# Kernel tuning notes

Hardware: AMD Instinct MI355X
Metric: run time of the kernel (lower is better)

## Reference

```python
import jax, jax.numpy as jnp
import numpy as np

N = 100000
E = 3200000
D = 256
HOPS = 3  # K + 1


def setup_inputs() -> dict:
    key = jax.random.key(0)
    k1, k2, k3, k4, k5 = jax.random.split(key, 5)
    node_features = jax.random.normal(k1, (N, D), dtype=jnp.float32)
    # glorot-uniform-like scale for K+1 Dense kernels
    limit = np.sqrt(6.0 / (D + D)).astype(np.float32)
    W = jax.random.uniform(k2, (HOPS, D, D), dtype=jnp.float32, minval=-limit, maxval=limit)
    adj_vals = jax.random.uniform(k3, (HOPS, E), dtype=jnp.float32)
    adj_rows = jax.random.randint(k4, (HOPS, E), 0, N, dtype=jnp.int32)
    adj_cols = jax.random.randint(k5, (HOPS, E), 0, N, dtype=jnp.int32)
    return {"node_features": node_features, "W": W, "adj_vals": adj_vals,
            "adj_rows": adj_rows, "adj_cols": adj_cols}


def reference(node_features, W, adj_vals, adj_rows, adj_cols):
    """Faithful eval-mode forward: sum over hops of SpMM(A_hop, X @ W_hop), then ReLU.
    Dropout is identity at inference (training=False)."""
    n = node_features.shape[0]
    out = jnp.zeros((n, W.shape[-1]), dtype=node_features.dtype)
    for hop in range(W.shape[0]):  # small fixed K+1 loop, structurally distinct hops
        feats = node_features @ W[hop]                      # [N, out_dim]
        msgs = adj_vals[hop][:, None] * feats[adj_cols[hop]]  # gather + scale, [E, out_dim]
        out = out + jax.ops.segment_sum(msgs, adj_rows[hop], num_segments=n)
    return jax.nn.relu(out)
```

## Files before the change

kernel.cpp:

```cpp
#include <hip/hip_runtime.h>

#define D 256
#define MAXKEY 1600
#define PCH 32768

typedef __attribute__((ext_vector_type(8))) short short8;
typedef __attribute__((ext_vector_type(4))) float f32x4;

__device__ __forceinline__ ushort f2b(float f) {
    unsigned u = __float_as_uint(f);
    u += 0x7fffu + ((u >> 16) & 1u);
    return (ushort)(u >> 16);
}
__device__ __forceinline__ float b2f(ushort h) {
    return __uint_as_float(((unsigned)h) << 16);
}
__device__ __forceinline__ long long ntload_ll(const void* p) {
    return __builtin_nontemporal_load((const long long*)p);
}

__global__ void zero_int_kernel(int* __restrict__ p, int n) {
    int stride = gridDim.x * blockDim.x;
    for (int i = blockIdx.x * blockDim.x + threadIdx.x; i < n; i += stride) p[i] = 0;
}

__global__ void xconv_kernel(const float* __restrict__ X, ushort* __restrict__ Xb, int total8) {
    int i = blockIdx.x * 256 + threadIdx.x;
    if (i >= total8) return;
    const float4 a = *(const float4*)(X + (size_t)i * 8);
    const float4 b = *(const float4*)(X + (size_t)i * 8 + 4);
    ushort o8[8] = {f2b(a.x), f2b(a.y), f2b(a.z), f2b(a.w),
                    f2b(b.x), f2b(b.y), f2b(b.z), f2b(b.w)};
    *(short8*)(Xb + (size_t)i * 8) = *(const short8*)o8;
}

__global__ void wconv_kernel(const float* __restrict__ W, ushort* __restrict__ WT, int total) {
    int idx = blockIdx.x * 256 + threadIdx.x;
    if (idx >= total) return;
    int h = idx >> 16;
    int c = (idx >> 8) & 255, k = idx & 255;
    WT[(h << 16) + c * 256 + k] = f2b(W[(h << 16) + k * 256 + c]);
}

__global__ __launch_bounds__(256) void bhist_kernel(const int* __restrict__ rows,
                                                    int* __restrict__ bhistG, int e, int nbuk) {
    __shared__ int lh[MAXKEY];
    int h = blockIdx.y;
    const int* r = rows + (size_t)h * e;
    for (int k = threadIdx.x; k < nbuk; k += 256) lh[k] = 0;
    __syncthreads();
    int stride = gridDim.x * 256;
    for (int i = blockIdx.x * 256 + threadIdx.x; i < e; i += stride)
        atomicAdd(&lh[r[i] >> 6], 1);
    __syncthreads();
    int* g = bhistG + (size_t)h * nbuk;
    for (int k = threadIdx.x; k < nbuk; k += 256)
        if (lh[k]) atomicAdd(&g[k], lh[k]);
}

__global__ __launch_bounds__(1024) void bscan_kernel(const int* __restrict__ bhistG,
                                                     int* __restrict__ gbase,
                                                     int* __restrict__ gcur, int total) {
    __shared__ int s[1024];
    int t = threadIdx.x;
    int C = (total + 1023) >> 10;
    int i0 = t * C, i1 = min(i0 + C, total);
    int sum = 0;
    for (int i = i0; i < i1; ++i) sum += bhistG[i];
    s[t] = sum;
    __syncthreads();
    for (int off = 1; off < 1024; off <<= 1) {
        int x = (t >= off) ? s[t - off] : 0;
        __syncthreads();
        s[t] += x;
        __syncthreads();
    }
    int run = s[t] - sum;
    for (int i = i0; i < i1; ++i) {
        gbase[i] = run; gcur[i] = run;
        run += bhistG[i];
    }
    if (t == 1023) gbase[total] = s[1023];
}

__global__ __launch_bounds__(256) void bpart_kernel(const int* __restrict__ rows,
                                                    const int* __restrict__ cols,
                                                    const float* __restrict__ vals,
                                                    int* __restrict__ gcur, int2* __restrict__ raw,
                                                    int e, int nbuk) {
    __shared__ int lbase[MAXKEY];
    __shared__ int lcur[MAXKEY];
    int h = blockIdx.y;
    const int*   rr = rows + (size_t)h * e;
    const int*   cc = cols + (size_t)h * e;
    const float* vv = vals + (size_t)h * e;
    int c0 = blockIdx.x * PCH;
    int c1 = min(c0 + PCH, e);
    if (c0 >= c1) return;
    for (int k = threadIdx.x; k < nbuk; k += 256) { lbase[k] = 0; lcur[k] = 0; }
    __syncthreads();
    for (int i = c0 + threadIdx.x; i < c1; i += 256)
        atomicAdd(&lbase[rr[i] >> 6], 1);
    __syncthreads();
    int* gc = gcur + (size_t)h * nbuk;
    for (int k = threadIdx.x; k < nbuk; k += 256) {
        int c = lbase[k];
        lbase[k] = c ? atomicAdd(&gc[k], c) : 0;
    }
    __syncthreads();
    for (int i = c0 + threadIdx.x; i < c1; i += 256) {
        int row = rr[i];
        int p = lbase[row >> 6] + atomicAdd(&lcur[row >> 6], 1);
        raw[p] = make_int2(cc[i] | ((row & 63) << 24), __float_as_int(vv[i]));
    }
}

__global__ __launch_bounds__(256) void bsort_kernel(const int* __restrict__ gbase,
                                                    const int2* __restrict__ raw,
                                                    int2* __restrict__ eg,
                                                    int* __restrict__ row_ptr,
                                                    int n, int nbuk) {
    __shared__ int hist[64], excl[64], cur[64];
    int key = blockIdx.x;
    int h = key / nbuk, b = key % nbuk;
    int s = gbase[key], t = gbase[key + 1];
    int tid = threadIdx.x;
    if (tid < 64) hist[tid] = 0;
    __syncthreads();
    for (int i = s + tid; i < t; i += 256)
        atomicAdd(&hist[(((unsigned)raw[i].x) >> 24) & 63], 1);
    __syncthreads();
    if (tid == 0) {
        int run = s;
        for (int j = 0; j < 64; ++j) { excl[j] = run; cur[j] = run; run += hist[j]; }
    }
    __syncthreads();
    int* rp = row_ptr + (size_t)h * (n + 1);
    if (tid < 64) {
        int grow = b * 64 + tid;
        if (grow < n) rp[grow] = excl[tid];
    }
    if (tid == 0 && b == nbuk - 1) rp[n] = t;
    for (int i = s + tid; i < t; i += 256) {
        int2 ev = raw[i];
        int j = (((unsigned)ev.x) >> 24) & 63;
        int p = atomicAdd(&cur[j], 1);
        eg[p] = ev;
    }
}

__global__ __launch_bounds__(256) void spmmX_kernel(const int* __restrict__ rp,
                                                    const int2* __restrict__ eg,
                                                    const ushort* __restrict__ Xb,
                                                    ushort* __restrict__ Yh, int n) {
    int w = threadIdx.x >> 6, lane = threadIdx.x & 63;
    int r = blockIdx.x * 4 + w;
    if (r >= n) return;
    int half = lane >> 5, l5 = lane & 31;
    int doff = l5 * 8;
    int e0 = rp[r], e1 = rp[r + 1];
    float acc[8] = {};
    int m0 = e0 + half, m1 = e0 + 2 + half;
    long long ev0 = (m0 < e1) ? ntload_ll(eg + m0) : 0;
    long long ev1 = (m1 < e1) ? ntload_ll(eg + m1) : 0;
    for (int ee = e0; ee < e1; ee += 4) {
        long long c0 = ev0, c1 = ev1;
        int n0 = ee + 4 + half, n1 = ee + 6 + half;
        ev0 = (n0 < e1) ? ntload_ll(eg + n0) : 0;
        ev1 = (n1 < e1) ? ntload_ll(eg + n1) : 0;
        int col0 = ((int)(unsigned)c0) & 0xFFFFFF;
        int col1 = ((int)(unsigned)c1) & 0xFFFFFF;
        short8 v0 = *(const short8*)(Xb + (size_t)col0 * 256 + doff);
        short8 v1 = *(const short8*)(Xb + (size_t)col1 * 256 + doff);
        float val0 = __int_as_float((int)(c0 >> 32));
        float val1 = __int_as_float((int)(c1 >> 32));
        #pragma unroll
        for (int i = 0; i < 8; ++i)
            acc[i] = fmaf(val0, b2f((ushort)v0[i]), acc[i]);
        #pragma unroll
        for (int i = 0; i < 8; ++i)
            acc[i] = fmaf(val1, b2f((ushort)v1[i]), acc[i]);
    }
    #pragma unroll
    for (int i = 0; i < 8; ++i)
        acc[i] += __shfl_xor(acc[i], 32);
    if (half == 0) {
        union { ushort u[8]; long long ll[2]; } o;
        #pragma unroll
        for (int i = 0; i < 8; ++i) o.u[i] = f2b(acc[i]);
        long long* dst = (long long*)(Yh + (size_t)r * 256 + doff);
        __builtin_nontemporal_store(o.ll[0], dst);
        __builtin_nontemporal_store(o.ll[1], dst + 1);
    }
}

#define APAD 40

__global__ __launch_bounds__(256) void gemmY_kernel(const ushort* __restrict__ Y,
                                                    const ushort* __restrict__ WT,
                                                    float* __restrict__ out, int M,
                                                    int nh, int mode) {
    __shared__ ushort As[64 * APAD];
    __shared__ ushort Bs[64 * APAD];
    int tid = threadIdx.x;
    int r0 = blockIdx.x * 64, c0 = blockIdx.y * 64;
    int w = tid >> 6, lane = tid & 63;
    int wr = w >> 1, wc = w & 1;
    int lo = lane & 15, hi = lane >> 4;
    f32x4 acc[2][2] = {};
    int srow = tid >> 2;
    int skoff = (tid & 3) * 8;
    int arow = r0 + srow; if (arow > M - 1) arow = M - 1;
    for (int h = 0; h < nh; ++h) {
        const ushort* ap = Y + ((size_t)h * M + arow) * 256 + skoff;
        const ushort* bp = WT + ((size_t)h << 16) + (size_t)(c0 + srow) * 256 + skoff;
        for (int kk = 0; kk < 256; kk += 32) {
            short8 av = *(const short8*)(ap + kk);
            short8 bv = *(const short8*)(bp + kk);
            __syncthreads();
            *(short8*)&As[srow * APAD + skoff] = av;
            *(short8*)&Bs[srow * APAD + skoff] = bv;
            __syncthreads();
            short8 a0 = *(const short8*)&As[(wr * 32 +      lo) * APAD + hi * 8];
            short8 a1 = *(const short8*)&As[(wr * 32 + 16 + lo) * APAD + hi * 8];
            short8 b0 = *(const short8*)&Bs[(wc * 32 +      lo) * APAD + hi * 8];
            short8 b1 = *(const short8*)&Bs[(wc * 32 + 16 + lo) * APAD + hi * 8];
            acc[0][0] = __builtin_amdgcn_mfma_f32_16x16x32_bf16(a0, b0, acc[0][0], 0, 0, 0);
            acc[0][1] = __builtin_amdgcn_mfma_f32_16x16x32_bf16(a0, b1, acc[0][1], 0, 0, 0);
            acc[1][0] = __builtin_amdgcn_mfma_f32_16x16x32_bf16(a1, b0, acc[1][0], 0, 0, 0);
            acc[1][1] = __builtin_amdgcn_mfma_f32_16x16x32_bf16(a1, b1, acc[1][1], 0, 0, 0);
        }
    }
    for (int mi = 0; mi < 2; ++mi)
        for (int ni = 0; ni < 2; ++ni)
            for (int i = 0; i < 4; ++i) {
                int row = r0 + wr * 32 + mi * 16 + hi * 4 + i;
                int col = c0 + wc * 32 + ni * 16 + lo;
                if (row < M) {
                    float v = acc[mi][ni][i];
                    float* op = &out[(size_t)row * 256 + col];
                    if (mode & 1) v += *op;
                    if (mode & 2) v = fmaxf(v, 0.f);
                    *op = v;
                }
            }
}

extern "C" void kernel_launch(void* const* d_in, const int* in_sizes, int n_in,
                              void* d_out, int out_size, void* d_ws, size_t ws_size,
                              hipStream_t stream) {
    const float* X    = (const float*)d_in[0];
    const float* W    = (const float*)d_in[1];
    const float* vals = (const float*)d_in[2];
    const int*   rows = (const int*)d_in[3];
    const int*   cols = (const int*)d_in[4];
    int n    = in_sizes[0] / D;
    int hops = in_sizes[1] / (D * D);
    int e    = in_sizes[2] / hops;

    int nbuk    = (n + 63) / 64;
    int nkeytot = hops * nbuk;
    int nchunks = (e + PCH - 1) / PCH;

    float* out = (float*)d_out;

    auto padded = [](size_t b) { return (b + 255) & ~(size_t)255; };
    char* wsb = (char*)d_ws;
    size_t off = 0;
    auto alloc = [&](size_t bytes) -> void* { void* p = wsb + off; off += padded(bytes); return p; };

    ushort* WT      = (ushort*)alloc((size_t)hops * D * D * 2);
    ushort* Xb      = (ushort*)alloc((size_t)n * D * 2);
    int*    bhistG  = (int*)   alloc((size_t)nkeytot * 4);
    int*    gbase   = (int*)   alloc((size_t)(nkeytot + 1) * 4);
    int*    gcur    = (int*)   alloc((size_t)nkeytot * 4);
    int2*   raw     = (int2*)  alloc((size_t)hops * e * 8);
    int2*   edges   = (int2*)  alloc((size_t)hops * e * 8);
    int*    row_ptr = (int*)   alloc((size_t)hops * (n + 1) * 4);
    ushort* Y       = (ushort*)raw;

    xconv_kernel<<<(n * D / 8 + 255) / 256, 256, 0, stream>>>(X, Xb, n * D / 8);
    wconv_kernel<<<(hops * D * D + 255) / 256, 256, 0, stream>>>(W, WT, hops * D * D);

    zero_int_kernel<<<(nkeytot + 255) / 256, 256, 0, stream>>>(bhistG, nkeytot);
    bhist_kernel<<<dim3(128, hops), 256, 0, stream>>>(rows, bhistG, e, nbuk);
    bscan_kernel<<<1, 1024, 0, stream>>>(bhistG, gbase, gcur, nkeytot);
    bpart_kernel<<<dim3(nchunks, hops), 256, 0, stream>>>(rows, cols, vals, gcur, raw, e, nbuk);
    bsort_kernel<<<nkeytot, 256, 0, stream>>>(gbase, raw, edges, row_ptr, n, nbuk);

    for (int h = 0; h < hops; ++h) {
        spmmX_kernel<<<(n + 3) / 4, 256, 0, stream>>>(row_ptr + (size_t)h * (n + 1), edges, Xb, Y, n);
        int mode = (h > 0 ? 1 : 0) | (h == hops - 1 ? 2 : 0);
        gemmY_kernel<<<dim3((n + 63) / 64, D / 64), 256, 0, stream>>>(Y, WT + (size_t)h * D * D,
                                                                      out, n, 1, mode);
    }
}
```

Before: 1.291 ms.

## Widen row buckets to 256 and fuse per-hop GEMMs into one multi-hop GEMM

Edge bucketing now uses 256-row buckets instead of 64, so the row offset is packed into bits 17-24 and the column into 17 bits. bsort replaces its serial 64-entry prefix with a parallel 256-entry scan. When the workspace is large enough, each hop's SpMM result is kept in its own Y buffer and a single gemmY call sums over all hops, removing the read-modify-write of the fp32 output between hops. The risks are that columns must fit in 17 bits (n up to 131072) and that the fused path needs a much larger workspace.

```diff
diff --git a/kernel.cpp b/kernel.cpp
--- a/kernel.cpp
+++ b/kernel.cpp
@@ -1,7 +1,7 @@
 #include <hip/hip_runtime.h>
 
 #define D 256
-#define MAXKEY 1600
+#define MAXB 512
 #define PCH 32768
 
 typedef __attribute__((ext_vector_type(8))) short short8;
@@ -44,14 +44,14 @@
 
 __global__ __launch_bounds__(256) void bhist_kernel(const int* __restrict__ rows,
                                                     int* __restrict__ bhistG, int e, int nbuk) {
-    __shared__ int lh[MAXKEY];
+    __shared__ int lh[MAXB];
     int h = blockIdx.y;
     const int* r = rows + (size_t)h * e;
     for (int k = threadIdx.x; k < nbuk; k += 256) lh[k] = 0;
     __syncthreads();
     int stride = gridDim.x * 256;
     for (int i = blockIdx.x * 256 + threadIdx.x; i < e; i += stride)
-        atomicAdd(&lh[r[i] >> 6], 1);
+        atomicAdd(&lh[r[i] >> 8], 1);
     __syncthreads();
     int* g = bhistG + (size_t)h * nbuk;
     for (int k = threadIdx.x; k < nbuk; k += 256)
@@ -88,8 +88,8 @@
                                                     const float* __restrict__ vals,
                                                     int* __restrict__ gcur, int2* __restrict__ raw,
                                                     int e, int nbuk) {
-    __shared__ int lbase[MAXKEY];
-    __shared__ int lcur[MAXKEY];
+    __shared__ int lbase[MAXB];
+    __shared__ int lcur[MAXB];
     int h = blockIdx.y;
     const int*   rr = rows + (size_t)h * e;
     const int*   cc = cols + (size_t)h * e;
@@ -100,7 +100,7 @@
     for (int k = threadIdx.x; k < nbuk; k += 256) { lbase[k] = 0; lcur[k] = 0; }
     __syncthreads();
     for (int i = c0 + threadIdx.x; i < c1; i += 256)
-        atomicAdd(&lbase[rr[i] >> 6], 1);
+        atomicAdd(&lbase[rr[i] >> 8], 1);
     __syncthreads();
     int* gc = gcur + (size_t)h * nbuk;
     for (int k = threadIdx.x; k < nbuk; k += 256) {
@@ -110,8 +110,9 @@
     __syncthreads();
     for (int i = c0 + threadIdx.x; i < c1; i += 256) {
         int row = rr[i];
-        int p = lbase[row >> 6] + atomicAdd(&lcur[row >> 6], 1);
-        raw[p] = make_int2(cc[i] | ((row & 63) << 24), __float_as_int(vv[i]));
+        int b = row >> 8;
+        int p = lbase[b] + atomicAdd(&lcur[b], 1);
+        raw[p] = make_int2(cc[i] | ((row & 255) << 17), __float_as_int(vv[i]));
     }
 }
 
@@ -120,30 +121,35 @@
                                                     int2* __restrict__ eg,
                                                     int* __restrict__ row_ptr,
                                                     int n, int nbuk) {
-    __shared__ int hist[64], excl[64], cur[64];
+    __shared__ int hist[256], ss[256], cur[256];
     int key = blockIdx.x;
     int h = key / nbuk, b = key % nbuk;
     int s = gbase[key], t = gbase[key + 1];
     int tid = threadIdx.x;
-    if (tid < 64) hist[tid] = 0;
+    hist[tid] = 0;
     __syncthreads();
     for (int i = s + tid; i < t; i += 256)
-        atomicAdd(&hist[(((unsigned)raw[i].x) >> 24) & 63], 1);
-    __syncthreads();
-    if (tid == 0) {
-        int run = s;
-        for (int j = 0; j < 64; ++j) { excl[j] = run; cur[j] = run; run += hist[j]; }
-    }
-    __syncthreads();
+        atomicAdd(&hist[(((unsigned)raw[i].x) >> 17) & 255], 1);
+    __syncthreads();
+    int v = hist[tid];
+    ss[tid] = v;
+    __syncthreads();
+    for (int off = 1; off < 256; off <<= 1) {
+        int x = (tid >= off) ? ss[tid - off] : 0;
+        __syncthreads();
+        ss[tid] += x;
+        __syncthreads();
+    }
+    int excl = s + ss[tid] - v;
+    cur[tid] = excl;
     int* rp = row_ptr + (size_t)h * (n + 1);
-    if (tid < 64) {
-        int grow = b * 64 + tid;
-        if (grow < n) rp[grow] = excl[tid];
-    }
-    if (tid == 0 && b == nbuk - 1) rp[n] = t;
+    int grow = b * 256 + tid;
+    if (grow < n) rp[grow] = excl;
+    if (tid == 255 && b == nbuk - 1) rp[n] = t;
+    __syncthreads();
     for (int i = s + tid; i < t; i += 256) {
         int2 ev = raw[i];
-        int j = (((unsigned)ev.x) >> 24) & 63;
+        int j = (((unsigned)ev.x) >> 17) & 255;
         int p = atomicAdd(&cur[j], 1);
         eg[p] = ev;
     }
@@ -168,8 +174,8 @@
         int n0 = ee + 4 + half, n1 = ee + 6 + half;
         ev0 = (n0 < e1) ? ntload_ll(eg + n0) : 0;
         ev1 = (n1 < e1) ? ntload_ll(eg + n1) : 0;
-        int col0 = ((int)(unsigned)c0) & 0xFFFFFF;
-        int col1 = ((int)(unsigned)c1) & 0xFFFFFF;
+        int col0 = ((int)(unsigned)c0) & 0x1FFFF;
+        int col1 = ((int)(unsigned)c1) & 0x1FFFF;
         short8 v0 = *(const short8*)(Xb + (size_t)col0 * 256 + doff);
         short8 v1 = *(const short8*)(Xb + (size_t)col1 * 256 + doff);
         float val0 = __int_as_float((int)(c0 >> 32));
@@ -258,7 +264,7 @@
     int hops = in_sizes[1] / (D * D);
     int e    = in_sizes[2] / hops;
 
-    int nbuk    = (n + 63) / 64;
+    int nbuk    = (n + 255) / 256;
     int nkeytot = hops * nbuk;
     int nchunks = (e + PCH - 1) / PCH;
 
@@ -274,10 +280,13 @@
     int*    bhistG  = (int*)   alloc((size_t)nkeytot * 4);
     int*    gbase   = (int*)   alloc((size_t)(nkeytot + 1) * 4);
     int*    gcur    = (int*)   alloc((size_t)nkeytot * 4);
+    int*    row_ptr = (int*)   alloc((size_t)hops * (n + 1) * 4);
+    int2*   edges   = (int2*)  alloc((size_t)hops * e * 8);
+    size_t  raw_off = off;
     int2*   raw     = (int2*)  alloc((size_t)hops * e * 8);
-    int2*   edges   = (int2*)  alloc((size_t)hops * e * 8);
-    int*    row_ptr = (int*)   alloc((size_t)hops * (n + 1) * 4);
-    ushort* Y       = (ushort*)raw;
+
+    bool bigY = (ws_size >= raw_off + (size_t)hops * n * D * 2);
+    ushort* Y = (ushort*)raw;
 
     xconv_kernel<<<(n * D / 8 + 255) / 256, 256, 0, stream>>>(X, Xb, n * D / 8);
     wconv_kernel<<<(hops * D * D + 255) / 256, 256, 0, stream>>>(W, WT, hops * D * D);
@@ -288,10 +297,18 @@
     bpart_kernel<<<dim3(nchunks, hops), 256, 0, stream>>>(rows, cols, vals, gcur, raw, e, nbuk);
     bsort_kernel<<<nkeytot, 256, 0, stream>>>(gbase, raw, edges, row_ptr, n, nbuk);
 
-    for (int h = 0; h < hops; ++h) {
-        spmmX_kernel<<<(n + 3) / 4, 256, 0, stream>>>(row_ptr + (size_t)h * (n + 1), edges, Xb, Y, n);
-        int mode = (h > 0 ? 1 : 0) | (h == hops - 1 ? 2 : 0);
-        gemmY_kernel<<<dim3((n + 63) / 64, D / 64), 256, 0, stream>>>(Y, WT + (size_t)h * D * D,
-                                                                      out, n, 1, mode);
-    }
-}
+    if (bigY) {
+        for (int h = 0; h < hops; ++h)
+            spmmX_kernel<<<(n + 3) / 4, 256, 0, stream>>>(row_ptr + (size_t)h * (n + 1), edges,
+                                                          Xb, Y + (size_t)h * n * D, n);
+        gemmY_kernel<<<dim3((n + 63) / 64, D / 64), 256, 0, stream>>>(Y, WT, out, n, hops, 2);
+    } else {
+        for (int h = 0; h < hops; ++h) {
+            spmmX_kernel<<<(n + 3) / 4, 256, 0, stream>>>(row_ptr + (size_t)h * (n + 1), edges,
+                                                          Xb, Y, n);
+            int mode = (h > 0 ? 1 : 0) | (h == hops - 1 ? 2 : 0);
+            gemmY_kernel<<<dim3((n + 63) / 64, D / 64), 256, 0, stream>>>(Y, WT + (size_t)h * D * D,
+                                                                          out, n, 1, mode);
+        }
+    }
+}
```

New measurement: 1.193 ms. 7.6% less time.
